# Kernel tuning notes

Hardware: AMD Instinct MI355X
Metric: run time of the kernel (lower is better)

## Reference

```python
import jax, jax.numpy as jnp
import numpy as np

B, L, N, C = 8, 33600, 128, 80
ALPHA, BETA, TOPK, EPS = 1.0, 6.0, 13, 1e-9


def setup_inputs() -> dict:
    key = jax.random.key(0)
    ks = jax.random.split(key, 7)
    pred_scores = jax.random.uniform(ks[0], (B, L, C), jnp.float32)  # post-sigmoid scores
    pc = jax.random.uniform(ks[1], (B, L, 2), jnp.float32) * 1024.0
    pwh = jax.random.uniform(ks[2], (B, L, 2), jnp.float32) * 128.0 + 8.0
    pred_boxes = jnp.concatenate([pc - pwh / 2, pc + pwh / 2], axis=-1)  # xyxy
    gc = jax.random.uniform(ks[3], (B, N, 2), jnp.float32) * 1024.0
    gwh = jax.random.uniform(ks[4], (B, N, 2), jnp.float32) * 256.0 + 16.0
    gt_boxes = jnp.concatenate([gc - gwh / 2, gc + gwh / 2], axis=-1)  # xyxy
    anchor_points = jax.random.uniform(ks[5], (1, L, 2), jnp.float32) * 1024.0
    gt_labels = jax.random.randint(ks[6], (B, N, 1), 0, C).astype(jnp.int64)
    # last quarter of GT slots are padding
    pad_gt_mask = (jnp.arange(N)[None, :, None] < 96).astype(jnp.float32)
    pad_gt_mask = jnp.broadcast_to(pad_gt_mask, (B, N, 1))
    return {"pred_scores": pred_scores, "pred_boxes": pred_boxes,
            "anchor_points": anchor_points, "gt_labels": gt_labels,
            "gt_boxes": gt_boxes, "pad_gt_mask": pad_gt_mask, "bg_index": C}


def _pairwise_iou(gt, pr):
    # gt: [B,N,4], pr: [B,L,4] xyxy -> iou [B,N,L]
    lt = jnp.maximum(gt[:, :, None, :2], pr[:, None, :, :2])
    rb = jnp.minimum(gt[:, :, None, 2:], pr[:, None, :, 2:])
    wh = jnp.clip(rb - lt, 0.0)
    inter = wh[..., 0] * wh[..., 1]
    area_g = ((gt[..., 2] - gt[..., 0]) * (gt[..., 3] - gt[..., 1]))[:, :, None]
    area_p = ((pr[..., 2] - pr[..., 0]) * (pr[..., 3] - pr[..., 1]))[:, None, :]
    iou = inter / (area_g + area_p - inter + EPS)
    iou = jnp.where(iou > 1.0 + EPS, 0.0, iou)
    return jnp.clip(jnp.nan_to_num(iou), 0.0, 1.0)


def reference(pred_scores, pred_boxes, anchor_points, gt_labels, gt_boxes, pad_gt_mask, bg_index):
    b, l, c = pred_scores.shape
    n = gt_boxes.shape[1]
    iou = _pairwise_iou(gt_boxes, pred_boxes)  # [B,N,L]

    # spatial containment of anchor points in horizontal gt boxes -> [B,N,L]
    pts = anchor_points[0]  # [L,2]
    spatial = ((pts[None, None, :, 0] >= gt_boxes[:, :, None, 0]) &
               (pts[None, None, :, 0] <= gt_boxes[:, :, None, 2]) &
               (pts[None, None, :, 1] >= gt_boxes[:, :, None, 1]) &
               (pts[None, None, :, 1] <= gt_boxes[:, :, None, 3]))

    # gather per-GT class scores: class_scores[b,n,l] = pred_scores[b,l,label[b,n]]
    lbl = jnp.clip(gt_labels[..., 0], 0, c - 1)  # [B,N]
    ps_t = jnp.transpose(pred_scores, (0, 2, 1))  # [B,C,L]
    class_scores = jnp.take_along_axis(ps_t, jnp.broadcast_to(lbl[:, :, None], (b, n, l)), axis=1)

    align = (class_scores ** ALPHA) * (iou ** BETA)  # [B,N,L]

    # top-k per GT over anchors
    k = min(TOPK, l)
    s = align * spatial.astype(align.dtype)
    _, topk_idx = jax.lax.top_k(s, k)  # [B,N,k]
    bidx = jnp.arange(b)[:, None, None]
    gidx = jnp.arange(n)[None, :, None]
    topk_mask = jnp.zeros((b, n, l), bool).at[bidx, gidx, topk_idx].set(True)
    topk_mask = topk_mask & (pad_gt_mask[..., 0] > 0)[:, :, None]

    positive = topk_mask.astype(align.dtype) * spatial.astype(align.dtype) * pad_gt_mask

    # conflict resolution: anchors matched to >1 GT keep only the best-IoU GT
    conflict = positive.sum(axis=1) > 1  # [B,L]
    best_gt = jnp.argmax(iou, axis=1)  # [B,L]
    best_mask = (jnp.arange(n)[None, :, None] == best_gt[:, None, :])  # [B,N,L]
    positive = jnp.where(conflict[:, None, :], positive * best_mask.astype(positive.dtype), positive)

    has_assign = positive.sum(axis=1) > 0  # [B,L]
    gt_idx = jnp.argmax(positive, axis=1)  # [B,L]
    assigned_labels = jnp.take_along_axis(gt_labels[..., 0], gt_idx, axis=1)  # [B,L]
    assigned_labels = jnp.where(has_assign, assigned_labels, bg_index)
    assigned_boxes = jnp.take_along_axis(gt_boxes, jnp.broadcast_to(gt_idx[:, :, None], (b, l, 4)), axis=1)

    masked_align = align * positive
    max_align = masked_align.max(axis=-1, keepdims=True)  # [B,N,1]
    max_iou = (iou * positive).max(axis=-1, keepdims=True)  # [B,N,1]
    norm_align = masked_align / (max_align + EPS) * max_iou
    norm_factor = norm_align.max(axis=1)  # [B,L]
    # scatter score at assigned class; bg labels (== C) one-hot to all-zero row
    assigned_scores = jax.nn.one_hot(assigned_labels, c, dtype=pred_scores.dtype)
    assigned_scores = assigned_scores * (norm_factor * has_assign.astype(norm_factor.dtype))[:, :, None]
    return assigned_labels, assigned_boxes, assigned_scores
```

## Files before the change

### kernel.cpp

```cpp
#include <hip/hip_runtime.h>
#include <cstdint>
#include <cstddef>

#define B_DIM 8
#define L_DIM 33600
#define N_DIM 128
#define C_DIM 80
#define K_TOP 13
#define EPS_F 1e-9f
#define NCHUNK 132
#define SEGSZ 96

__device__ __forceinline__ float iou_pair(float g0, float g1, float g2, float g3,
                                          float p0, float p1, float p2, float p3) {
    float ltx = fmaxf(g0, p0), lty = fmaxf(g1, p1);
    float rbx = fminf(g2, p2), rby = fminf(g3, p3);
    float wx = fmaxf(__fsub_rn(rbx, ltx), 0.0f);
    float wy = fmaxf(__fsub_rn(rby, lty), 0.0f);
    float inter = __fmul_rn(wx, wy);
    float ag = __fmul_rn(__fsub_rn(g2, g0), __fsub_rn(g3, g1));
    float ap = __fmul_rn(__fsub_rn(p2, p0), __fsub_rn(p3, p1));
    float den = __fadd_rn(__fsub_rn(__fadd_rn(ag, ap), inter), EPS_F);
    float iou = __fdiv_rn(inter, den);
    if (iou > 1.0f) iou = 0.0f;
    iou = fminf(fmaxf(iou, 0.0f), 1.0f);
    return iou;
}

__device__ __forceinline__ unsigned long long make_key(double s, int l) {
    unsigned long long sb = (unsigned long long)__double_as_longlong(s);
    return (sb & 0xFFFFFFFFFFFF0000ull) | (unsigned long long)(0xFFFF - l);
}

__global__ __launch_bounds__(256) void k_push(
    const float* __restrict__ pts, const float* __restrict__ gbox,
    const float* __restrict__ gpad,
    int* __restrict__ scount, unsigned short* __restrict__ bucket,
    ulonglong2* __restrict__ spat, ulonglong2* __restrict__ posb2,
    float* __restrict__ maxal, float* __restrict__ maxio)
{
    const int chunk = blockIdx.x, b = blockIdx.y, t = threadIdx.x;
    __shared__ float4 gb[N_DIM];
    __shared__ float  gp[N_DIM];
    __shared__ int    lcnt[N_DIM];
    if (t < N_DIM) {
        gb[t] = reinterpret_cast<const float4*>(gbox)[(size_t)b * N_DIM + t];
        gp[t] = gpad[b * N_DIM + t];
        lcnt[t] = 0;
        if (chunk == 0) { maxal[b * N_DIM + t] = 0.0f; maxio[b * N_DIM + t] = 0.0f; }
    }
    __syncthreads();

    const int l = chunk * 256 + t;
    const bool inrange = (l < L_DIM);

    if (inrange) {
        posb2[(size_t)b * L_DIM + l] = make_ulonglong2(0ull, 0ull);
        const float2 ap = reinterpret_cast<const float2*>(pts)[l];
        unsigned long long m0 = 0ull, m1 = 0ull;
        for (int n = 0; n < N_DIM; ++n) {
            if (gp[n] <= 0.0f) continue;
            const float4 g = gb[n];
            bool in = (ap.x >= g.x && ap.x <= g.z && ap.y >= g.y && ap.y <= g.w);
            if (n < 64) m0 |= in ? (1ull << n) : 0ull;
            else        m1 |= in ? (1ull << (n - 64)) : 0ull;
        }
        spat[(size_t)b * L_DIM + l] = make_ulonglong2(m0, m1);
        if (l >= 32) {
            const size_t segbase = ((size_t)(b * N_DIM) * NCHUNK + chunk) * SEGSZ;
            unsigned long long m = m0;
            while (m) {
                int n = __ffsll((long long)m) - 1; m &= m - 1;
                int pos = atomicAdd(&lcnt[n], 1);
                if (pos < SEGSZ) bucket[segbase + (size_t)n * NCHUNK * SEGSZ + pos] = (unsigned short)l;
            }
            m = m1;
            while (m) {
                int n = __ffsll((long long)m) - 1; m &= m - 1;
                int pos = atomicAdd(&lcnt[n + 64], 1);
                if (pos < SEGSZ) bucket[segbase + (size_t)(n + 64) * NCHUNK * SEGSZ + pos] = (unsigned short)l;
            }
        }
    }
    __syncthreads();

    if (t < N_DIM)
        scount[(b * N_DIM + t) * NCHUNK + chunk] = min(lcnt[t], SEGSZ);
}

__global__ __launch_bounds__(256) void k_top13(
    const float* __restrict__ psc, const float* __restrict__ pbox,
    const float* __restrict__ pts, const int* __restrict__ glbl,
    const float* __restrict__ gbox, const float* __restrict__ gpad,
    const int* __restrict__ scount, const unsigned short* __restrict__ bucket,
    unsigned long long* __restrict__ posbits)
{
    const int n = blockIdx.x, b = blockIdx.y, t = threadIdx.x;
    if (gpad[b * N_DIM + n] <= 0.0f) return;

    const float g0 = gbox[(b * N_DIM + n) * 4 + 0];
    const float g1 = gbox[(b * N_DIM + n) * 4 + 1];
    const float g2 = gbox[(b * N_DIM + n) * 4 + 2];
    const float g3 = gbox[(b * N_DIM + n) * 4 + 3];
    int lbl = glbl[b * N_DIM + n];
    lbl = min(max(lbl, 0), C_DIM - 1);
    const float* psb = psc + (size_t)b * L_DIM * C_DIM;
    const float* pbb = pbox + (size_t)b * L_DIM * 4;
    const int bn = b * N_DIM + n;

    __shared__ int pfx[NCHUNK + 1];
    if (t < NCHUNK) pfx[t + 1] = scount[bn * NCHUNK + t];
    __syncthreads();
    if (t == 0) { pfx[0] = 0; for (int i = 1; i <= NCHUNK; ++i) pfx[i] += pfx[i - 1]; }
    __syncthreads();
    const int nc = pfx[NCHUNK];
    const unsigned short* seg = bucket + (size_t)bn * NCHUNK * SEGSZ;

    unsigned long long key[K_TOP];
    #pragma unroll
    for (int k = 0; k < K_TOP; ++k) key[k] = 0ull;

    for (int i = t; i < nc + 32; i += 256) {
        int l;
        if (i < 32) l = i;
        else {
            const int ci = i - 32;
            int lo = 0, hi = NCHUNK - 1;
            while (lo < hi) { int mid = (lo + hi + 1) >> 1; if (pfx[mid] <= ci) lo = mid; else hi = mid - 1; }
            l = (int)seg[(size_t)lo * SEGSZ + (ci - pfx[lo])];
        }
        const float2 ap = reinterpret_cast<const float2*>(pts)[l];
        unsigned long long ck = (unsigned long long)(0xFFFF - l);
        if (ap.x >= g0 && ap.x <= g2 && ap.y >= g1 && ap.y <= g3) {
            const float4 pbv = reinterpret_cast<const float4*>(pbb)[l];
            float iou = iou_pair(g0, g1, g2, g3, pbv.x, pbv.y, pbv.z, pbv.w);
            if (iou > 0.0f) {
                float cs = psb[(size_t)l * C_DIM + lbl];
                double d = (double)iou, d2 = d * d;
                ck = make_key((double)cs * (d2 * d2 * d2), l);
            }
        }
        if (ck > key[K_TOP - 1]) {
            #pragma unroll
            for (int k = 0; k < K_TOP; ++k) {
                unsigned long long hi = key[k] > ck ? key[k] : ck;
                unsigned long long lo = key[k] > ck ? ck : key[k];
                key[k] = hi; ck = lo;
            }
        }
    }

    const int lane = t & 63, wid = t >> 6;
    __shared__ unsigned long long wl[4 * K_TOP];
    #pragma unroll 1
    for (int r = 0; r < K_TOP; ++r) {
        unsigned long long best = key[0];
        #pragma unroll
        for (int d = 1; d < 64; d <<= 1) {
            unsigned long long o = __shfl_xor(best, d, 64);
            best = o > best ? o : best;
        }
        if (key[0] == best && best != 0ull) {
            #pragma unroll
            for (int k = 0; k < K_TOP - 1; ++k) key[k] = key[k + 1];
            key[K_TOP - 1] = 0ull;
        }
        if (lane == 0) wl[wid * K_TOP + r] = best;
    }
    __syncthreads();
    if (wid != 0) return;

    unsigned long long v = (lane < 4 * K_TOP) ? wl[lane] : 0ull;
    #pragma unroll 1
    for (int r = 0; r < K_TOP; ++r) {
        unsigned long long best = v;
        #pragma unroll
        for (int d = 1; d < 64; d <<= 1) {
            unsigned long long o = __shfl_xor(best, d, 64);
            best = o > best ? o : best;
        }
        if (v == best) v = 0ull;
        if (lane == 0) {
            int win = 0xFFFF - (int)(best & 0xFFFFull);
            atomicOr(&posbits[((size_t)b * L_DIM + win) * 2 + (n >> 6)],
                     1ULL << (n & 63));
        }
    }
}

__global__ __launch_bounds__(256) void k_assign(
    const float* __restrict__ psc, const float* __restrict__ pbox,
    const int* __restrict__ glbl, const float* __restrict__ gbox,
    const unsigned long long* __restrict__ posbits,
    const ulonglong2* __restrict__ spat,
    const int* __restrict__ bgp,
    float* __restrict__ out_lab, float* __restrict__ out_box,
    int* __restrict__ fin_out, float* __restrict__ alat,
    float* __restrict__ maxal, float* __restrict__ maxio)
{
    const int b = blockIdx.y, t = threadIdx.x;
    const int l = blockIdx.x * 256 + t;
    __shared__ float4 gb[N_DIM];
    __shared__ int    gl[N_DIM];
    __shared__ int    qlist[256];
    __shared__ int    qn;
    if (t == 0) qn = 0;
    if (t < N_DIM) {
        gb[t] = reinterpret_cast<const float4*>(gbox)[(size_t)b * N_DIM + t];
        gl[t] = glbl[b * N_DIM + t];
    }
    __syncthreads();

    if (l < L_DIM) {
        const size_t bl = (size_t)b * L_DIM + l;
        const unsigned long long w0 = posbits[bl * 2 + 0];
        const unsigned long long w1 = posbits[bl * 2 + 1];
        const ulonglong2 sm = spat[bl];
        const unsigned long long p0 = w0 & sm.x, p1 = w1 & sm.y;
        const int pcnt = __popcll(p0) + __popcll(p1);

        if (pcnt <= 1) {
            int fin = (pcnt == 1) ? (p0 ? (__ffsll(p0) - 1) : (64 + __ffsll(p1) - 1)) : -1;
            out_lab[bl] = (fin >= 0) ? (float)gl[fin] : (float)bgp[0];
            int gidx = (fin >= 0) ? fin : 0;
            reinterpret_cast<float4*>(out_box)[bl] = gb[gidx];
            fin_out[bl] = fin;
            if (fin >= 0) {
                const float4 pb = reinterpret_cast<const float4*>(pbox)[bl];
                float4 g = gb[fin];
                float iou = iou_pair(g.x, g.y, g.z, g.w, pb.x, pb.y, pb.z, pb.w);
                int lb = min(max(gl[fin], 0), C_DIM - 1);
                float cs = psc[bl * C_DIM + lb];
                float al = cs * powf(iou, 6.0f);
                alat[bl] = al;
                atomicMax((int*)&maxal[b * N_DIM + fin], __float_as_int(al));
                atomicMax((int*)&maxio[b * N_DIM + fin], __float_as_int(iou));
            }
        } else {
            qlist[atomicAdd(&qn, 1)] = l;
        }
    }
    __syncthreads();

    const int lane = t & 63, wid = t >> 6;
    const int nq = qn;
    for (int i = wid; i < nq; i += 4) {
        const int ql = qlist[i];
        const size_t bl = (size_t)b * L_DIM + ql;
        const float4 pb = reinterpret_cast<const float4*>(pbox)[bl];
        float4 gA = gb[lane];
        float4 gB = gb[lane + 64];
        float iouA = iou_pair(gA.x, gA.y, gA.z, gA.w, pb.x, pb.y, pb.z, pb.w);
        float iouB = iou_pair(gB.x, gB.y, gB.z, gB.w, pb.x, pb.y, pb.z, pb.w);
        unsigned long long kA = ((unsigned long long)__float_as_uint(iouA) << 32)
                              | (unsigned long long)(0xFFFFFFFFu - (unsigned)lane);
        unsigned long long kB = ((unsigned long long)__float_as_uint(iouB) << 32)
                              | (unsigned long long)(0xFFFFFFFFu - (unsigned)(lane + 64));
        unsigned long long k = kA > kB ? kA : kB;
        #pragma unroll
        for (int d = 1; d < 64; d <<= 1) {
            unsigned long long o = __shfl_xor(k, d, 64);
            k = o > k ? o : k;
        }
        if (lane == 0) {
            int bestn = (int)(0xFFFFFFFFu - (unsigned)(k & 0xFFFFFFFFull));
            float bestiou = __uint_as_float((unsigned)(k >> 32));
            const unsigned long long w0 = posbits[bl * 2 + 0];
            const unsigned long long w1 = posbits[bl * 2 + 1];
            const ulonglong2 sm = spat[bl];
            const unsigned long long p0 = w0 & sm.x, p1 = w1 & sm.y;
            bool posbest = (bestn < 64) ? ((p0 >> bestn) & 1ull) : ((p1 >> (bestn - 64)) & 1ull);
            int fin = posbest ? bestn : -1;
            out_lab[bl] = (fin >= 0) ? (float)gl[fin] : (float)bgp[0];
            int gidx = (fin >= 0) ? fin : 0;
            reinterpret_cast<float4*>(out_box)[bl] = gb[gidx];
            fin_out[bl] = fin;
            if (fin >= 0) {
                int lb = min(max(gl[fin], 0), C_DIM - 1);
                float cs = psc[bl * C_DIM + lb];
                float al = cs * powf(bestiou, 6.0f);
                alat[bl] = al;
                atomicMax((int*)&maxal[b * N_DIM + fin], __float_as_int(al));
                atomicMax((int*)&maxio[b * N_DIM + fin], __float_as_int(bestiou));
            }
        }
    }
}

__global__ __launch_bounds__(256) void k_out(
    const int* __restrict__ fin_out, const float* __restrict__ alat,
    const float* __restrict__ maxal, const float* __restrict__ maxio,
    const int* __restrict__ glbl,
    float* __restrict__ outs)
{
    const int APB = 16;
    const int a0 = blockIdx.x * APB;
    const int t = threadIdx.x;
    __shared__ float snf[APB];
    __shared__ int   scl[APB];
    if (t < APB) {
        int a = a0 + t;
        float v = 0.0f; int c = -1;
        if (a < B_DIM * L_DIM) {
            int b = a / L_DIM;
            int fin = fin_out[a];
            if (fin >= 0) {
                v = alat[a] / (maxal[b * N_DIM + fin] + EPS_F) * maxio[b * N_DIM + fin];
                c = glbl[b * N_DIM + fin];
            }
        }
        snf[t] = v; scl[t] = c;
    }
    __syncthreads();
    float4* out4 = reinterpret_cast<float4*>(outs);
    for (int j = t; j < APB * 20; j += 256) {
        int ai = j / 20;
        int a = a0 + ai;
        if (a >= B_DIM * L_DIM) continue;
        int c0 = (j - ai * 20) * 4;
        float v = snf[ai]; int cl = scl[ai];
        float4 o;
        o.x = (c0 + 0 == cl) ? v : 0.0f;
        o.y = (c0 + 1 == cl) ? v : 0.0f;
        o.z = (c0 + 2 == cl) ? v : 0.0f;
        o.w = (c0 + 3 == cl) ? v : 0.0f;
        out4[(size_t)a * 20 + (j - ai * 20)] = o;
    }
}

extern "C" void kernel_launch(void* const* d_in, const int* in_sizes, int n_in,
                              void* d_out, int out_size, void* d_ws, size_t ws_size,
                              hipStream_t stream)
{
    const float* psc  = (const float*)d_in[0];
    const float* pbox = (const float*)d_in[1];
    const float* pts  = (const float*)d_in[2];
    const int*   glbl = (const int*)d_in[3];
    const float* gbox = (const float*)d_in[4];
    const float* gpad = (const float*)d_in[5];
    const int*   bgp  = (const int*)d_in[6];

    const size_t P = (size_t)B_DIM * L_DIM * 2 * sizeof(unsigned long long);
    char* w = (char*)d_ws;
    unsigned long long* posbits = (unsigned long long*)w;
    float* maxal = (float*)(w + P);
    float* maxio = (float*)(w + P + 4096);
    int*   scount = (int*) (w + P + 8192);
    ulonglong2* spat = (ulonglong2*)(w + P + 8192 + 540672);
    int*   fin   = (int*)  (w + 2 * P + 8192 + 540672);
    float* alat  = (float*)(w + 2 * P + 8192 + 540672 + 1075200);
    unsigned short* bucket = (unsigned short*)(w + 2 * P + 8192 + 540672 + 2 * 1075200);

    float* out_lab = (float*)d_out;
    float* out_box = out_lab + (size_t)B_DIM * L_DIM;
    float* out_sc  = out_box + (size_t)B_DIM * L_DIM * 4;

    k_push<<<dim3(NCHUNK, B_DIM), dim3(256), 0, stream>>>(
        pts, gbox, gpad, scount, bucket, spat, (ulonglong2*)posbits, maxal, maxio);
    k_top13<<<dim3(N_DIM, B_DIM), dim3(256), 0, stream>>>(
        psc, pbox, pts, glbl, gbox, gpad, scount, bucket, posbits);
    k_assign<<<dim3((L_DIM + 255) / 256, B_DIM), dim3(256), 0, stream>>>(
        psc, pbox, glbl, gbox, posbits, spat, bgp,
        out_lab, out_box, fin, alat, maxal, maxio);
    k_out<<<dim3((B_DIM * L_DIM + 15) / 16), dim3(256), 0, stream>>>(
        fin, alat, maxal, maxio, glbl, out_sc);
}
```

Before: 91.16 us.

## Process two anchors per thread in push, parallel prefix scan, nontemporal output stores

The push kernel now handles 512 anchors per block, two per thread, with half as many chunks and larger segments. Padded GT boxes are turned into empty boxes so the containment loop needs no branch. The top-13 kernel replaces its serial prefix sum over chunk counts with a parallel Hillis-Steele scan. Output label, box and score writes use nontemporal stores to keep streaming data out of the cache. The risks are higher register pressure in push and more synchronisation steps in the scan.

```diff
diff --git a/kernel.cpp b/kernel.cpp
--- a/kernel.cpp
+++ b/kernel.cpp
@@ -8,8 +8,10 @@
 #define C_DIM 80
 #define K_TOP 13
 #define EPS_F 1e-9f
-#define NCHUNK 132
-#define SEGSZ 96
+#define NCH2 66
+#define SEGSZ 128
+
+typedef float f32x4 __attribute__((ext_vector_type(4)));
 
 __device__ __forceinline__ float iou_pair(float g0, float g1, float g2, float g3,
                                           float p0, float p1, float p2, float p3) {
@@ -32,6 +34,10 @@
     return (sb & 0xFFFFFFFFFFFF0000ull) | (unsigned long long)(0xFFFF - l);
 }
 
+__device__ __forceinline__ void nt_store4(float4 v, float4* p) {
+    __builtin_nontemporal_store(*(f32x4*)&v, (f32x4*)p);
+}
+
 __global__ __launch_bounds__(256) void k_push(
     const float* __restrict__ pts, const float* __restrict__ gbox,
     const float* __restrict__ gpad,
@@ -41,51 +47,74 @@
 {
     const int chunk = blockIdx.x, b = blockIdx.y, t = threadIdx.x;
     __shared__ float4 gb[N_DIM];
-    __shared__ float  gp[N_DIM];
     __shared__ int    lcnt[N_DIM];
     if (t < N_DIM) {
-        gb[t] = reinterpret_cast<const float4*>(gbox)[(size_t)b * N_DIM + t];
-        gp[t] = gpad[b * N_DIM + t];
+        float4 g = reinterpret_cast<const float4*>(gbox)[(size_t)b * N_DIM + t];
+        if (gpad[b * N_DIM + t] <= 0.0f) g = make_float4(3e38f, 3e38f, -3e38f, -3e38f);
+        gb[t] = g;
         lcnt[t] = 0;
         if (chunk == 0) { maxal[b * N_DIM + t] = 0.0f; maxio[b * N_DIM + t] = 0.0f; }
     }
     __syncthreads();
 
-    const int l = chunk * 256 + t;
-    const bool inrange = (l < L_DIM);
-
-    if (inrange) {
-        posb2[(size_t)b * L_DIM + l] = make_ulonglong2(0ull, 0ull);
-        const float2 ap = reinterpret_cast<const float2*>(pts)[l];
-        unsigned long long m0 = 0ull, m1 = 0ull;
-        for (int n = 0; n < N_DIM; ++n) {
-            if (gp[n] <= 0.0f) continue;
-            const float4 g = gb[n];
-            bool in = (ap.x >= g.x && ap.x <= g.z && ap.y >= g.y && ap.y <= g.w);
-            if (n < 64) m0 |= in ? (1ull << n) : 0ull;
-            else        m1 |= in ? (1ull << (n - 64)) : 0ull;
-        }
-        spat[(size_t)b * L_DIM + l] = make_ulonglong2(m0, m1);
-        if (l >= 32) {
-            const size_t segbase = ((size_t)(b * N_DIM) * NCHUNK + chunk) * SEGSZ;
-            unsigned long long m = m0;
-            while (m) {
-                int n = __ffsll((long long)m) - 1; m &= m - 1;
-                int pos = atomicAdd(&lcnt[n], 1);
-                if (pos < SEGSZ) bucket[segbase + (size_t)n * NCHUNK * SEGSZ + pos] = (unsigned short)l;
-            }
-            m = m1;
-            while (m) {
-                int n = __ffsll((long long)m) - 1; m &= m - 1;
-                int pos = atomicAdd(&lcnt[n + 64], 1);
-                if (pos < SEGSZ) bucket[segbase + (size_t)(n + 64) * NCHUNK * SEGSZ + pos] = (unsigned short)l;
-            }
+    const int l0 = chunk * 512 + t, l1 = l0 + 256;
+    const bool v0 = (l0 < L_DIM), v1 = (l1 < L_DIM);
+    float a0x = -3e38f, a0y = -3e38f, a1x = -3e38f, a1y = -3e38f;
+    if (v0) {
+        posb2[(size_t)b * L_DIM + l0] = make_ulonglong2(0ull, 0ull);
+        const float2 ap = reinterpret_cast<const float2*>(pts)[l0];
+        a0x = ap.x; a0y = ap.y;
+    }
+    if (v1) {
+        posb2[(size_t)b * L_DIM + l1] = make_ulonglong2(0ull, 0ull);
+        const float2 ap = reinterpret_cast<const float2*>(pts)[l1];
+        a1x = ap.x; a1y = ap.y;
+    }
+
+    unsigned long long m0a = 0ull, m1a = 0ull, m0b = 0ull, m1b = 0ull;
+    for (int n = 0; n < N_DIM; ++n) {
+        const float4 g = gb[n];
+        bool i0 = (a0x >= g.x && a0x <= g.z && a0y >= g.y && a0y <= g.w);
+        bool i1 = (a1x >= g.x && a1x <= g.z && a1y >= g.y && a1y <= g.w);
+        if (n < 64) { m0a |= i0 ? (1ull << n) : 0ull;        m0b |= i1 ? (1ull << n) : 0ull; }
+        else        { m1a |= i0 ? (1ull << (n - 64)) : 0ull; m1b |= i1 ? (1ull << (n - 64)) : 0ull; }
+    }
+    if (v0) spat[(size_t)b * L_DIM + l0] = make_ulonglong2(m0a, m1a);
+    if (v1) spat[(size_t)b * L_DIM + l1] = make_ulonglong2(m0b, m1b);
+
+    const size_t segbase = ((size_t)(b * N_DIM) * NCH2 + chunk) * SEGSZ;
+    if (v0 && l0 >= 32) {
+        unsigned long long m = m0a;
+        while (m) {
+            int n = __ffsll((long long)m) - 1; m &= m - 1;
+            int pos = atomicAdd(&lcnt[n], 1);
+            if (pos < SEGSZ) bucket[segbase + (size_t)n * NCH2 * SEGSZ + pos] = (unsigned short)l0;
+        }
+        m = m1a;
+        while (m) {
+            int n = __ffsll((long long)m) - 1; m &= m - 1;
+            int pos = atomicAdd(&lcnt[n + 64], 1);
+            if (pos < SEGSZ) bucket[segbase + (size_t)(n + 64) * NCH2 * SEGSZ + pos] = (unsigned short)l0;
+        }
+    }
+    if (v1) {
+        unsigned long long m = m0b;
+        while (m) {
+            int n = __ffsll((long long)m) - 1; m &= m - 1;
+            int pos = atomicAdd(&lcnt[n], 1);
+            if (pos < SEGSZ) bucket[segbase + (size_t)n * NCH2 * SEGSZ + pos] = (unsigned short)l1;
+        }
+        m = m1b;
+        while (m) {
+            int n = __ffsll((long long)m) - 1; m &= m - 1;
+            int pos = atomicAdd(&lcnt[n + 64], 1);
+            if (pos < SEGSZ) bucket[segbase + (size_t)(n + 64) * NCH2 * SEGSZ + pos] = (unsigned short)l1;
         }
     }
     __syncthreads();
 
     if (t < N_DIM)
-        scount[(b * N_DIM + t) * NCHUNK + chunk] = min(lcnt[t], SEGSZ);
+        scount[(b * N_DIM + t) * NCH2 + chunk] = min(lcnt[t], SEGSZ);
 }
 
 __global__ __launch_bounds__(256) void k_top13(
@@ -108,13 +137,23 @@
     const float* pbb = pbox + (size_t)b * L_DIM * 4;
     const int bn = b * N_DIM + n;
 
-    __shared__ int pfx[NCHUNK + 1];
-    if (t < NCHUNK) pfx[t + 1] = scount[bn * NCHUNK + t];
-    __syncthreads();
-    if (t == 0) { pfx[0] = 0; for (int i = 1; i <= NCHUNK; ++i) pfx[i] += pfx[i - 1]; }
-    __syncthreads();
-    const int nc = pfx[NCHUNK];
-    const unsigned short* seg = bucket + (size_t)bn * NCHUNK * SEGSZ;
+    __shared__ int pfx[NCH2 + 1];
+    __shared__ int tmp[128];
+    if (t < 128) tmp[t] = (t < NCH2) ? scount[bn * NCH2 + t] : 0;
+    __syncthreads();
+    #pragma unroll
+    for (int off = 1; off < 128; off <<= 1) {
+        int v = 0;
+        if (t < 128) { v = tmp[t]; if (t >= off) v += tmp[t - off]; }
+        __syncthreads();
+        if (t < 128) tmp[t] = v;
+        __syncthreads();
+    }
+    if (t < NCH2) pfx[t + 1] = tmp[t];
+    if (t == 0) pfx[0] = 0;
+    __syncthreads();
+    const int nc = pfx[NCH2];
+    const unsigned short* seg = bucket + (size_t)bn * NCH2 * SEGSZ;
 
     unsigned long long key[K_TOP];
     #pragma unroll
@@ -125,7 +164,7 @@
         if (i < 32) l = i;
         else {
             const int ci = i - 32;
-            int lo = 0, hi = NCHUNK - 1;
+            int lo = 0, hi = NCH2 - 1;
             while (lo < hi) { int mid = (lo + hi + 1) >> 1; if (pfx[mid] <= ci) lo = mid; else hi = mid - 1; }
             l = (int)seg[(size_t)lo * SEGSZ + (ci - pfx[lo])];
         }
@@ -221,9 +260,9 @@
 
         if (pcnt <= 1) {
             int fin = (pcnt == 1) ? (p0 ? (__ffsll(p0) - 1) : (64 + __ffsll(p1) - 1)) : -1;
-            out_lab[bl] = (fin >= 0) ? (float)gl[fin] : (float)bgp[0];
+            __builtin_nontemporal_store((fin >= 0) ? (float)gl[fin] : (float)bgp[0], &out_lab[bl]);
             int gidx = (fin >= 0) ? fin : 0;
-            reinterpret_cast<float4*>(out_box)[bl] = gb[gidx];
+            nt_store4(gb[gidx], &reinterpret_cast<float4*>(out_box)[bl]);
             fin_out[bl] = fin;
             if (fin >= 0) {
                 const float4 pb = reinterpret_cast<const float4*>(pbox)[bl];
@@ -271,9 +310,9 @@
             const unsigned long long p0 = w0 & sm.x, p1 = w1 & sm.y;
             bool posbest = (bestn < 64) ? ((p0 >> bestn) & 1ull) : ((p1 >> (bestn - 64)) & 1ull);
             int fin = posbest ? bestn : -1;
-            out_lab[bl] = (fin >= 0) ? (float)gl[fin] : (float)bgp[0];
+            __builtin_nontemporal_store((fin >= 0) ? (float)gl[fin] : (float)bgp[0], &out_lab[bl]);
             int gidx = (fin >= 0) ? fin : 0;
-            reinterpret_cast<float4*>(out_box)[bl] = gb[gidx];
+            nt_store4(gb[gidx], &reinterpret_cast<float4*>(out_box)[bl]);
             fin_out[bl] = fin;
             if (fin >= 0) {
                 int lb = min(max(gl[fin], 0), C_DIM - 1);
@@ -324,7 +363,7 @@
         o.y = (c0 + 1 == cl) ? v : 0.0f;
         o.z = (c0 + 2 == cl) ? v : 0.0f;
         o.w = (c0 + 3 == cl) ? v : 0.0f;
-        out4[(size_t)a * 20 + (j - ai * 20)] = o;
+        nt_store4(o, &out4[(size_t)a * 20 + (j - ai * 20)]);
     }
 }
 
@@ -346,16 +385,16 @@
     float* maxal = (float*)(w + P);
     float* maxio = (float*)(w + P + 4096);
     int*   scount = (int*) (w + P + 8192);
-    ulonglong2* spat = (ulonglong2*)(w + P + 8192 + 540672);
-    int*   fin   = (int*)  (w + 2 * P + 8192 + 540672);
-    float* alat  = (float*)(w + 2 * P + 8192 + 540672 + 1075200);
-    unsigned short* bucket = (unsigned short*)(w + 2 * P + 8192 + 540672 + 2 * 1075200);
+    ulonglong2* spat = (ulonglong2*)(w + P + 8192 + 270336);
+    int*   fin   = (int*)  (w + 2 * P + 8192 + 270336);
+    float* alat  = (float*)(w + 2 * P + 8192 + 270336 + 1075200);
+    unsigned short* bucket = (unsigned short*)(w + 2 * P + 8192 + 270336 + 2 * 1075200);
 
     float* out_lab = (float*)d_out;
     float* out_box = out_lab + (size_t)B_DIM * L_DIM;
     float* out_sc  = out_box + (size_t)B_DIM * L_DIM * 4;
 
-    k_push<<<dim3(NCHUNK, B_DIM), dim3(256), 0, stream>>>(
+    k_push<<<dim3(NCH2, B_DIM), dim3(256), 0, stream>>>(
         pts, gbox, gpad, scount, bucket, spat, (ulonglong2*)posbits, maxal, maxio);
     k_top13<<<dim3(N_DIM, B_DIM), dim3(256), 0, stream>>>(
         psc, pbox, pts, glbl, gbox, gpad, scount, bucket, posbits);
```

Measured after the change: 90.90 us. About the same (-0.3%).
